# Kernel tuning notes

Measured on AMD Instinct MI355X. Metric: run time of the kernel, lower is better.

Reference implementation:

```python
import jax, jax.numpy as jnp
import numpy as np


def setup_inputs() -> dict:
    key = jax.random.key(0)
    ks = jax.random.split(key, 8)
    B = 32768
    return {
        "x": jax.random.normal(ks[0], (B, 784), dtype=jnp.float32),
        "conv_w": jax.random.normal(ks[1], (3, 3), dtype=jnp.float32),
        "fc1_w": jax.random.normal(ks[2], (512, 676), dtype=jnp.float32) * 0.04,
        "fc1_b": jax.random.normal(ks[3], (512,), dtype=jnp.float32),
        "fc2_w": jax.random.normal(ks[4], (512, 512), dtype=jnp.float32) * 0.04,
        "fc2_b": jax.random.normal(ks[5], (512,), dtype=jnp.float32),
        "out_w": jax.random.normal(ks[6], (10, 512), dtype=jnp.float32) * 0.04,
        "out_b": jax.random.normal(ks[7], (10,), dtype=jnp.float32),
    }


def reference(x, conv_w, fc1_w, fc1_b, fc2_w, fc2_b, out_w, out_b):
    B = x.shape[0]
    img = x.reshape(B, 1, 28, 28)  # NCHW, single channel
    # Valid 3x3 cross-correlation (same math as the nested tensordot loop).
    kern = conv_w.reshape(1, 1, 3, 3)  # OIHW
    conv = jax.lax.conv_general_dilated(
        img, kern, window_strides=(1, 1), padding="VALID",
        dimension_numbers=("NCHW", "OIHW", "NCHW"))  # [B,1,26,26]
    h = conv.reshape(B, 26 * 26)
    h = jax.nn.relu(h @ fc1_w.T + fc1_b)
    h = jax.nn.relu(h @ fc2_w.T + fc2_b)
    return h @ out_w.T + out_b  # [B,10] logits
```

## Files before the change

kernel.cpp:

```cpp
#include <hip/hip_runtime.h>

typedef unsigned short ushort_t;
typedef __attribute__((ext_vector_type(8))) short bf16x8;
typedef __attribute__((ext_vector_type(4))) float f32x4;
typedef __attribute__((ext_vector_type(16))) float f32x16;

__device__ __forceinline__ unsigned short f2bf(float f) {
    union { float f; unsigned u; } v; v.f = f;
    unsigned r = v.u + 0x7FFFu + ((v.u >> 16) & 1u);
    return (unsigned short)(r >> 16);
}

__global__ __launch_bounds__(256) void prep_w(const float* __restrict__ fc1_w,
                                              const float* __restrict__ cw,
                                              const float* __restrict__ fc2_w,
                                              const float* __restrict__ out_w,
                                              ushort_t* __restrict__ W1,
                                              ushort_t* __restrict__ W2,
                                              ushort_t* __restrict__ W3) {
    const int idx = blockIdx.x * 256 + threadIdx.x;
    if (idx < 425984) {
        const int ngrp = idx / 26624;
        const int kfrag = (idx % 26624) >> 9;
        const int li = idx & 511;
        const int lane = li >> 3, e = li & 7;
        const int n = ngrp * 32 + (lane & 31);
        const int p = kfrag * 16 + (lane >> 5) * 8 + e;
        float acc = 0.f;
        if (p < 784) {
            const int pr = p / 28, pc = p % 28;
#pragma unroll
            for (int dr = 0; dr < 3; ++dr) {
                const int r = pr - dr;
                if (r < 0 || r >= 26) continue;
#pragma unroll
                for (int dc = 0; dc < 3; ++dc) {
                    const int col = pc - dc;
                    if (col < 0 || col >= 26) continue;
                    acc += cw[dr * 3 + dc] * fc1_w[n * 676 + r * 26 + col];
                }
            }
        }
        W1[idx] = f2bf(acc);
    }
    if (idx < 262144) {
        const int ngrp = idx / 16384;
        const int kfrag = (idx % 16384) >> 9;
        const int li = idx & 511;
        const int lane = li >> 3, e = li & 7;
        const int n = ngrp * 32 + (lane & 31);
        const int p = kfrag * 16 + (lane >> 5) * 8 + e;
        W2[idx] = f2bf(fc2_w[n * 512 + p]);
    }
    if (idx < 16 * 512)  W3[idx] = (idx < 10 * 512) ? f2bf(out_w[idx]) : (ushort_t)0;
}

__global__ __launch_bounds__(512, 4) void mega5(const float* __restrict__ x,
                                                const ushort_t* __restrict__ W1,
                                                const ushort_t* __restrict__ W2,
                                                const ushort_t* __restrict__ W3,
                                                const float* __restrict__ b1,
                                                const float* __restrict__ b2,
                                                const float* __restrict__ ob,
                                                float* __restrict__ out) {
    extern __shared__ ushort_t smem[];
    ushort_t* xs0 = smem;
    ushort_t* hs  = smem + 4096;

    const int tid = threadIdx.x;
    const int wave = tid >> 6, lane = tid & 63;
    const int r32 = lane & 31, khalf = lane >> 5;
    const int xrow = tid >> 3, xoct = tid & 7;
    const int m0 = blockIdx.x * 64;
    const size_t ng0 = wave * 2, ng1 = wave * 2 + 1;

    f32x16 acc[2][2];
#pragma unroll
    for (int a = 0; a < 2; ++a)
#pragma unroll
        for (int j = 0; j < 2; ++j)
#pragma unroll
            for (int e = 0; e < 16; ++e) acc[a][j][e] = 0.f;

    f32x4 xv0, xv1;
    auto load_x = [&](int ks) {
        const int gc = ks * 64 + xoct * 8;
        if (gc < 784) {
            const f32x4* p = (const f32x4*)&x[(size_t)(m0 + xrow) * 784 + gc];
            xv0 = __builtin_nontemporal_load(p);
            xv1 = __builtin_nontemporal_load(p + 1);
        } else {
            xv0 = (f32x4){0.f, 0.f, 0.f, 0.f};
            xv1 = (f32x4){0.f, 0.f, 0.f, 0.f};
        }
    };
    auto store_x = [&](ushort_t* buf) {
        bf16x8 xv;
        xv[0] = (short)f2bf(xv0.x); xv[1] = (short)f2bf(xv0.y);
        xv[2] = (short)f2bf(xv0.z); xv[3] = (short)f2bf(xv0.w);
        xv[4] = (short)f2bf(xv1.x); xv[5] = (short)f2bf(xv1.y);
        xv[6] = (short)f2bf(xv1.z); xv[7] = (short)f2bf(xv1.w);
        *(bf16x8*)&buf[xrow * 64 + ((xoct ^ (xrow & 7)) * 8)] = xv;
    };

    auto write_h = [&](const float* __restrict__ bias) {
#pragma unroll
        for (int j = 0; j < 2; ++j) {
            const int n = (wave * 2 + j) * 32 + r32;
            const float bb = bias[n];
            const int nseg = n >> 3, nrem = n & 7;
#pragma unroll
            for (int i = 0; i < 2; ++i)
#pragma unroll
                for (int reg = 0; reg < 16; ++reg) {
                    const int m = i * 32 + 4 * khalf + (reg & 3) + 8 * (reg >> 2);
                    hs[m * 512 + ((nseg ^ (m & 7)) * 8) + nrem] = f2bf(fmaxf(acc[i][j][reg] + bb, 0.f));
                }
        }
    };

    load_x(0);
    store_x(xs0);
    __syncthreads();

    for (int ks = 0; ks < 12; ++ks) {
        load_x(ks + 1);
        const ushort_t* bufp = (ks & 1) ? hs : xs0;
#pragma unroll
        for (int ksub = 0; ksub < 4; ++ksub) {
            const int kfrag = ks * 4 + ksub;
            const bf16x8 bw0 = *(const bf16x8*)&W1[(ng0 * 52 + kfrag) * 512 + lane * 8];
            const bf16x8 bw1 = *(const bf16x8*)&W1[(ng1 * 52 + kfrag) * 512 + lane * 8];
            const int q = 2 * ksub + khalf;
            bf16x8 af[2];
#pragma unroll
            for (int i = 0; i < 2; ++i) {
                const int m = i * 32 + r32;
                af[i] = *(const bf16x8*)&bufp[m * 64 + ((q ^ (m & 7)) * 8)];
            }
            __builtin_amdgcn_s_setprio(1);
            acc[0][0] = __builtin_amdgcn_mfma_f32_32x32x16_bf16(af[0], bw0, acc[0][0], 0, 0, 0);
            acc[0][1] = __builtin_amdgcn_mfma_f32_32x32x16_bf16(af[0], bw1, acc[0][1], 0, 0, 0);
            acc[1][0] = __builtin_amdgcn_mfma_f32_32x32x16_bf16(af[1], bw0, acc[1][0], 0, 0, 0);
            acc[1][1] = __builtin_amdgcn_mfma_f32_32x32x16_bf16(af[1], bw1, acc[1][1], 0, 0, 0);
            __builtin_amdgcn_s_setprio(0);
        }
        store_x((ks & 1) ? xs0 : hs);
        __syncthreads();
    }
    {
        const ushort_t* bufp = xs0;
        const int kfrag = 48;
        const bf16x8 bw0 = *(const bf16x8*)&W1[(ng0 * 52 + kfrag) * 512 + lane * 8];
        const bf16x8 bw1 = *(const bf16x8*)&W1[(ng1 * 52 + kfrag) * 512 + lane * 8];
        const int q = khalf;
        bf16x8 af[2];
#pragma unroll
        for (int i = 0; i < 2; ++i) {
            const int m = i * 32 + r32;
            af[i] = *(const bf16x8*)&bufp[m * 64 + ((q ^ (m & 7)) * 8)];
        }
        __builtin_amdgcn_s_setprio(1);
        acc[0][0] = __builtin_amdgcn_mfma_f32_32x32x16_bf16(af[0], bw0, acc[0][0], 0, 0, 0);
        acc[0][1] = __builtin_amdgcn_mfma_f32_32x32x16_bf16(af[0], bw1, acc[0][1], 0, 0, 0);
        acc[1][0] = __builtin_amdgcn_mfma_f32_32x32x16_bf16(af[1], bw0, acc[1][0], 0, 0, 0);
        acc[1][1] = __builtin_amdgcn_mfma_f32_32x32x16_bf16(af[1], bw1, acc[1][1], 0, 0, 0);
        __builtin_amdgcn_s_setprio(0);
    }

    write_h(b1);
#pragma unroll
    for (int a = 0; a < 2; ++a)
#pragma unroll
        for (int j = 0; j < 2; ++j)
#pragma unroll
            for (int e = 0; e < 16; ++e) acc[a][j][e] = 0.f;
    __syncthreads();

    for (int ks = 0; ks < 8; ++ks) {
#pragma unroll
        for (int ksub = 0; ksub < 4; ++ksub) {
            const int kfrag = ks * 4 + ksub;
            const bf16x8 bw0 = *(const bf16x8*)&W2[(ng0 * 32 + kfrag) * 512 + lane * 8];
            const bf16x8 bw1 = *(const bf16x8*)&W2[(ng1 * 32 + kfrag) * 512 + lane * 8];
            const int hq = ks * 8 + 2 * ksub + khalf;
            bf16x8 af[2];
#pragma unroll
            for (int i = 0; i < 2; ++i) {
                const int m = i * 32 + r32;
                af[i] = *(const bf16x8*)&hs[m * 512 + ((hq ^ (m & 7)) * 8)];
            }
            __builtin_amdgcn_s_setprio(1);
            acc[0][0] = __builtin_amdgcn_mfma_f32_32x32x16_bf16(af[0], bw0, acc[0][0], 0, 0, 0);
            acc[0][1] = __builtin_amdgcn_mfma_f32_32x32x16_bf16(af[0], bw1, acc[0][1], 0, 0, 0);
            acc[1][0] = __builtin_amdgcn_mfma_f32_32x32x16_bf16(af[1], bw0, acc[1][0], 0, 0, 0);
            acc[1][1] = __builtin_amdgcn_mfma_f32_32x32x16_bf16(af[1], bw1, acc[1][1], 0, 0, 0);
            __builtin_amdgcn_s_setprio(0);
        }
    }
    __syncthreads();

    write_h(b2);
    __syncthreads();

    if (wave < 4) {
        const int quad = lane >> 4, l16 = lane & 15;
        const int row = wave * 16 + l16;
        f32x4 hacc = {0.f, 0.f, 0.f, 0.f};
#pragma unroll
        for (int ks = 0; ks < 16; ++ks) {
            const int seg = 4 * ks + quad;
            const bf16x8 a = *(const bf16x8*)&hs[row * 512 + ((seg ^ (row & 7)) * 8)];
            const bf16x8 b = *(const bf16x8*)&W3[l16 * 512 + ks * 32 + quad * 8];
            hacc = __builtin_amdgcn_mfma_f32_16x16x32_bf16(a, b, hacc, 0, 0, 0);
        }
        if (l16 < 10) {
            const float bb = ob[l16];
#pragma unroll
            for (int r = 0; r < 4; ++r)
                out[(size_t)(m0 + wave * 16 + quad * 4 + r) * 10 + l16] = hacc[r] + bb;
        }
    }
}

extern "C" void kernel_launch(void* const* d_in, const int* in_sizes, int n_in,
                              void* d_out, int out_size, void* d_ws, size_t ws_size,
                              hipStream_t stream) {
    const float* x      = (const float*)d_in[0];
    const float* conv_w = (const float*)d_in[1];
    const float* fc1_w  = (const float*)d_in[2];
    const float* fc1_b  = (const float*)d_in[3];
    const float* fc2_w  = (const float*)d_in[4];
    const float* fc2_b  = (const float*)d_in[5];
    const float* out_w  = (const float*)d_in[6];
    const float* out_b  = (const float*)d_in[7];
    float* out = (float*)d_out;

    ushort_t* W1 = (ushort_t*)d_ws;
    ushort_t* W2 = W1 + 425984;
    ushort_t* W3 = W2 + 262144;

    prep_w<<<dim3(1664), 256, 0, stream>>>(fc1_w, conv_w, fc2_w, out_w, W1, W2, W3);

    mega5<<<dim3(512), 512, 73728, stream>>>(x, W1, W2, W3, fc1_b, fc2_b, out_b, out);
}
```

Baseline: 216.8 us.

## Double the per-block row tile to 128 and batch weight fragment loads

Each block now processes 128 batch rows instead of 64: 4x2 accumulator tiles per wave, a wider x staging load per thread, double-size LDS buffers, and 256 blocks instead of 512. Every W1/W2 fragment fetched from global memory is reused across twice as many rows, halving total weight traffic. The weight fragments for a k-step are also loaded into registers together before the MFMA loop. The cost is one 144KB-LDS block per CU, meaning fewer resident waves to hide latency, plus much higher register pressure from 128 accumulator floats per lane.

```diff
diff --git a/kernel.cpp b/kernel.cpp
--- a/kernel.cpp
+++ b/kernel.cpp
@@ -55,7 +55,7 @@
     if (idx < 16 * 512)  W3[idx] = (idx < 10 * 512) ? f2bf(out_w[idx]) : (ushort_t)0;
 }
 
-__global__ __launch_bounds__(512, 4) void mega5(const float* __restrict__ x,
+__global__ __launch_bounds__(512, 2) void mega6(const float* __restrict__ x,
                                                 const ushort_t* __restrict__ W1,
                                                 const ushort_t* __restrict__ W2,
                                                 const ushort_t* __restrict__ W3,
@@ -65,42 +65,52 @@
                                                 float* __restrict__ out) {
     extern __shared__ ushort_t smem[];
     ushort_t* xs0 = smem;
-    ushort_t* hs  = smem + 4096;
+    ushort_t* hs  = smem + 8192;
 
     const int tid = threadIdx.x;
     const int wave = tid >> 6, lane = tid & 63;
     const int r32 = lane & 31, khalf = lane >> 5;
-    const int xrow = tid >> 3, xoct = tid & 7;
-    const int m0 = blockIdx.x * 64;
+    const int xrow = tid >> 2, xquad = tid & 3;
+    const int m0 = blockIdx.x * 128;
     const size_t ng0 = wave * 2, ng1 = wave * 2 + 1;
 
-    f32x16 acc[2][2];
-#pragma unroll
-    for (int a = 0; a < 2; ++a)
+    f32x16 acc[4][2];
+#pragma unroll
+    for (int a = 0; a < 4; ++a)
 #pragma unroll
         for (int j = 0; j < 2; ++j)
 #pragma unroll
             for (int e = 0; e < 16; ++e) acc[a][j][e] = 0.f;
 
-    f32x4 xv0, xv1;
+    f32x4 xv0, xv1, xv2, xv3;
     auto load_x = [&](int ks) {
-        const int gc = ks * 64 + xoct * 8;
+        const int gc = ks * 64 + xquad * 16;
         if (gc < 784) {
             const f32x4* p = (const f32x4*)&x[(size_t)(m0 + xrow) * 784 + gc];
             xv0 = __builtin_nontemporal_load(p);
             xv1 = __builtin_nontemporal_load(p + 1);
+            xv2 = __builtin_nontemporal_load(p + 2);
+            xv3 = __builtin_nontemporal_load(p + 3);
         } else {
             xv0 = (f32x4){0.f, 0.f, 0.f, 0.f};
             xv1 = (f32x4){0.f, 0.f, 0.f, 0.f};
+            xv2 = (f32x4){0.f, 0.f, 0.f, 0.f};
+            xv3 = (f32x4){0.f, 0.f, 0.f, 0.f};
         }
     };
     auto store_x = [&](ushort_t* buf) {
-        bf16x8 xv;
-        xv[0] = (short)f2bf(xv0.x); xv[1] = (short)f2bf(xv0.y);
-        xv[2] = (short)f2bf(xv0.z); xv[3] = (short)f2bf(xv0.w);
-        xv[4] = (short)f2bf(xv1.x); xv[5] = (short)f2bf(xv1.y);
-        xv[6] = (short)f2bf(xv1.z); xv[7] = (short)f2bf(xv1.w);
-        *(bf16x8*)&buf[xrow * 64 + ((xoct ^ (xrow & 7)) * 8)] = xv;
+        bf16x8 a, b;
+        a[0] = (short)f2bf(xv0.x); a[1] = (short)f2bf(xv0.y);
+        a[2] = (short)f2bf(xv0.z); a[3] = (short)f2bf(xv0.w);
+        a[4] = (short)f2bf(xv1.x); a[5] = (short)f2bf(xv1.y);
+        a[6] = (short)f2bf(xv1.z); a[7] = (short)f2bf(xv1.w);
+        b[0] = (short)f2bf(xv2.x); b[1] = (short)f2bf(xv2.y);
+        b[2] = (short)f2bf(xv2.z); b[3] = (short)f2bf(xv2.w);
+        b[4] = (short)f2bf(xv3.x); b[5] = (short)f2bf(xv3.y);
+        b[6] = (short)f2bf(xv3.z); b[7] = (short)f2bf(xv3.w);
+        const int o0 = xquad * 2;
+        *(bf16x8*)&buf[xrow * 64 + ((o0 ^ (xrow & 7)) * 8)] = a;
+        *(bf16x8*)&buf[xrow * 64 + (((o0 + 1) ^ (xrow & 7)) * 8)] = b;
     };
 
     auto write_h = [&](const float* __restrict__ bias) {
@@ -110,7 +120,7 @@
             const float bb = bias[n];
             const int nseg = n >> 3, nrem = n & 7;
 #pragma unroll
-            for (int i = 0; i < 2; ++i)
+            for (int i = 0; i < 4; ++i)
 #pragma unroll
                 for (int reg = 0; reg < 16; ++reg) {
                     const int m = i * 32 + 4 * khalf + (reg & 3) + 8 * (reg >> 2);
@@ -124,25 +134,30 @@
     __syncthreads();
 
     for (int ks = 0; ks < 12; ++ks) {
+        bf16x8 bw[4][2];
+#pragma unroll
+        for (int ksub = 0; ksub < 4; ++ksub) {
+            const int kfrag = ks * 4 + ksub;
+            bw[ksub][0] = *(const bf16x8*)&W1[(ng0 * 52 + kfrag) * 512 + lane * 8];
+            bw[ksub][1] = *(const bf16x8*)&W1[(ng1 * 52 + kfrag) * 512 + lane * 8];
+        }
         load_x(ks + 1);
         const ushort_t* bufp = (ks & 1) ? hs : xs0;
 #pragma unroll
         for (int ksub = 0; ksub < 4; ++ksub) {
-            const int kfrag = ks * 4 + ksub;
-            const bf16x8 bw0 = *(const bf16x8*)&W1[(ng0 * 52 + kfrag) * 512 + lane * 8];
-            const bf16x8 bw1 = *(const bf16x8*)&W1[(ng1 * 52 + kfrag) * 512 + lane * 8];
             const int q = 2 * ksub + khalf;
-            bf16x8 af[2];
-#pragma unroll
-            for (int i = 0; i < 2; ++i) {
+            bf16x8 af[4];
+#pragma unroll
+            for (int i = 0; i < 4; ++i) {
                 const int m = i * 32 + r32;
                 af[i] = *(const bf16x8*)&bufp[m * 64 + ((q ^ (m & 7)) * 8)];
             }
             __builtin_amdgcn_s_setprio(1);
-            acc[0][0] = __builtin_amdgcn_mfma_f32_32x32x16_bf16(af[0], bw0, acc[0][0], 0, 0, 0);
-            acc[0][1] = __builtin_amdgcn_mfma_f32_32x32x16_bf16(af[0], bw1, acc[0][1], 0, 0, 0);
-            acc[1][0] = __builtin_amdgcn_mfma_f32_32x32x16_bf16(af[1], bw0, acc[1][0], 0, 0, 0);
-            acc[1][1] = __builtin_amdgcn_mfma_f32_32x32x16_bf16(af[1], bw1, acc[1][1], 0, 0, 0);
+#pragma unroll
+            for (int i = 0; i < 4; ++i) {
+                acc[i][0] = __builtin_amdgcn_mfma_f32_32x32x16_bf16(af[i], bw[ksub][0], acc[i][0], 0, 0, 0);
+                acc[i][1] = __builtin_amdgcn_mfma_f32_32x32x16_bf16(af[i], bw[ksub][1], acc[i][1], 0, 0, 0);
+            }
             __builtin_amdgcn_s_setprio(0);
         }
         store_x((ks & 1) ? xs0 : hs);
@@ -150,27 +165,27 @@
     }
     {
         const ushort_t* bufp = xs0;
-        const int kfrag = 48;
-        const bf16x8 bw0 = *(const bf16x8*)&W1[(ng0 * 52 + kfrag) * 512 + lane * 8];
-        const bf16x8 bw1 = *(const bf16x8*)&W1[(ng1 * 52 + kfrag) * 512 + lane * 8];
+        bf16x8 bw0 = *(const bf16x8*)&W1[(ng0 * 52 + 48) * 512 + lane * 8];
+        bf16x8 bw1 = *(const bf16x8*)&W1[(ng1 * 52 + 48) * 512 + lane * 8];
         const int q = khalf;
-        bf16x8 af[2];
-#pragma unroll
-        for (int i = 0; i < 2; ++i) {
+        bf16x8 af[4];
+#pragma unroll
+        for (int i = 0; i < 4; ++i) {
             const int m = i * 32 + r32;
             af[i] = *(const bf16x8*)&bufp[m * 64 + ((q ^ (m & 7)) * 8)];
         }
         __builtin_amdgcn_s_setprio(1);
-        acc[0][0] = __builtin_amdgcn_mfma_f32_32x32x16_bf16(af[0], bw0, acc[0][0], 0, 0, 0);
-        acc[0][1] = __builtin_amdgcn_mfma_f32_32x32x16_bf16(af[0], bw1, acc[0][1], 0, 0, 0);
-        acc[1][0] = __builtin_amdgcn_mfma_f32_32x32x16_bf16(af[1], bw0, acc[1][0], 0, 0, 0);
-        acc[1][1] = __builtin_amdgcn_mfma_f32_32x32x16_bf16(af[1], bw1, acc[1][1], 0, 0, 0);
+#pragma unroll
+        for (int i = 0; i < 4; ++i) {
+            acc[i][0] = __builtin_amdgcn_mfma_f32_32x32x16_bf16(af[i], bw0, acc[i][0], 0, 0, 0);
+            acc[i][1] = __builtin_amdgcn_mfma_f32_32x32x16_bf16(af[i], bw1, acc[i][1], 0, 0, 0);
+        }
         __builtin_amdgcn_s_setprio(0);
     }
 
     write_h(b1);
 #pragma unroll
-    for (int a = 0; a < 2; ++a)
+    for (int a = 0; a < 4; ++a)
 #pragma unroll
         for (int j = 0; j < 2; ++j)
 #pragma unroll
@@ -178,23 +193,28 @@
     __syncthreads();
 
     for (int ks = 0; ks < 8; ++ks) {
+        bf16x8 bw[4][2];
 #pragma unroll
         for (int ksub = 0; ksub < 4; ++ksub) {
             const int kfrag = ks * 4 + ksub;
-            const bf16x8 bw0 = *(const bf16x8*)&W2[(ng0 * 32 + kfrag) * 512 + lane * 8];
-            const bf16x8 bw1 = *(const bf16x8*)&W2[(ng1 * 32 + kfrag) * 512 + lane * 8];
+            bw[ksub][0] = *(const bf16x8*)&W2[(ng0 * 32 + kfrag) * 512 + lane * 8];
+            bw[ksub][1] = *(const bf16x8*)&W2[(ng1 * 32 + kfrag) * 512 + lane * 8];
+        }
+#pragma unroll
+        for (int ksub = 0; ksub < 4; ++ksub) {
             const int hq = ks * 8 + 2 * ksub + khalf;
-            bf16x8 af[2];
-#pragma unroll
-            for (int i = 0; i < 2; ++i) {
+            bf16x8 af[4];
+#pragma unroll
+            for (int i = 0; i < 4; ++i) {
                 const int m = i * 32 + r32;
                 af[i] = *(const bf16x8*)&hs[m * 512 + ((hq ^ (m & 7)) * 8)];
             }
             __builtin_amdgcn_s_setprio(1);
-            acc[0][0] = __builtin_amdgcn_mfma_f32_32x32x16_bf16(af[0], bw0, acc[0][0], 0, 0, 0);
-            acc[0][1] = __builtin_amdgcn_mfma_f32_32x32x16_bf16(af[0], bw1, acc[0][1], 0, 0, 0);
-            acc[1][0] = __builtin_amdgcn_mfma_f32_32x32x16_bf16(af[1], bw0, acc[1][0], 0, 0, 0);
-            acc[1][1] = __builtin_amdgcn_mfma_f32_32x32x16_bf16(af[1], bw1, acc[1][1], 0, 0, 0);
+#pragma unroll
+            for (int i = 0; i < 4; ++i) {
+                acc[i][0] = __builtin_amdgcn_mfma_f32_32x32x16_bf16(af[i], bw[ksub][0], acc[i][0], 0, 0, 0);
+                acc[i][1] = __builtin_amdgcn_mfma_f32_32x32x16_bf16(af[i], bw[ksub][1], acc[i][1], 0, 0, 0);
+            }
             __builtin_amdgcn_s_setprio(0);
         }
     }
@@ -203,7 +223,7 @@
     write_h(b2);
     __syncthreads();
 
-    if (wave < 4) {
+    {
         const int quad = lane >> 4, l16 = lane & 15;
         const int row = wave * 16 + l16;
         f32x4 hacc = {0.f, 0.f, 0.f, 0.f};
@@ -242,5 +262,5 @@
 
     prep_w<<<dim3(1664), 256, 0, stream>>>(fc1_w, conv_w, fc2_w, out_w, W1, W2, W3);
 
-    mega5<<<dim3(512), 512, 73728, stream>>>(x, W1, W2, W3, fc1_b, fc2_b, out_b, out);
-}
+    mega6<<<dim3(256), 512, 147456, stream>>>(x, W1, W2, W3, fc1_b, fc2_b, out_b, out);
+}
```

New measurement: 228.9 us. +5.6%, slower.

## Double block to 128 rows with 1024 threads, load x directly into MFMA fragments

Applied to the files above, without the earlier changes.

The fused MLP kernel now handles 128 rows per block using 16 waves, two groups of 8 along M sharing each weight tile. The x staging through LDS and its per-step barriers are removed: each lane loads its fp32 A-fragment straight from global memory and converts it with the packed bf16 convert instruction. This cuts LDS traffic and synchronisation and halves the number of blocks. In exchange the x loads become strided per-lane fp32 reads with no prefetch, the block needs 128KB of LDS, and only 256 blocks are launched.

```diff
diff --git a/kernel.cpp b/kernel.cpp
--- a/kernel.cpp
+++ b/kernel.cpp
@@ -9,6 +9,12 @@
     union { float f; unsigned u; } v; v.f = f;
     unsigned r = v.u + 0x7FFFu + ((v.u >> 16) & 1u);
     return (unsigned short)(r >> 16);
+}
+
+__device__ __forceinline__ unsigned cvt_pk_bf16(float a, float b) {
+    unsigned r;
+    asm("v_cvt_pk_bf16_f32 %0, %1, %2" : "=v"(r) : "v"(a), "v"(b));
+    return r;
 }
 
 __global__ __launch_bounds__(256) void prep_w(const float* __restrict__ fc1_w,
@@ -55,24 +61,27 @@
     if (idx < 16 * 512)  W3[idx] = (idx < 10 * 512) ? f2bf(out_w[idx]) : (ushort_t)0;
 }
 
-__global__ __launch_bounds__(512, 4) void mega5(const float* __restrict__ x,
-                                                const ushort_t* __restrict__ W1,
-                                                const ushort_t* __restrict__ W2,
-                                                const ushort_t* __restrict__ W3,
-                                                const float* __restrict__ b1,
-                                                const float* __restrict__ b2,
-                                                const float* __restrict__ ob,
-                                                float* __restrict__ out) {
+__global__ __launch_bounds__(1024, 4) void mega7(const float* __restrict__ x,
+                                                 const ushort_t* __restrict__ W1,
+                                                 const ushort_t* __restrict__ W2,
+                                                 const ushort_t* __restrict__ W3,
+                                                 const float* __restrict__ b1,
+                                                 const float* __restrict__ b2,
+                                                 const float* __restrict__ ob,
+                                                 float* __restrict__ out) {
     extern __shared__ ushort_t smem[];
-    ushort_t* xs0 = smem;
-    ushort_t* hs  = smem + 4096;
+    ushort_t* hs = smem;
 
     const int tid = threadIdx.x;
     const int wave = tid >> 6, lane = tid & 63;
     const int r32 = lane & 31, khalf = lane >> 5;
-    const int xrow = tid >> 3, xoct = tid & 7;
-    const int m0 = blockIdx.x * 64;
-    const size_t ng0 = wave * 2, ng1 = wave * 2 + 1;
+    const int wm = wave >> 3;
+    const int wn = wave & 7;
+    const size_t ng0 = wn * 2, ng1 = wn * 2 + 1;
+    const int m0 = blockIdx.x * 128;
+
+    const float* xr0 = x + (size_t)(m0 + wm * 64 + r32) * 784 + khalf * 8;
+    const float* xr1 = xr0 + (size_t)32 * 784;
 
     f32x16 acc[2][2];
 #pragma unroll
@@ -82,89 +91,60 @@
 #pragma unroll
             for (int e = 0; e < 16; ++e) acc[a][j][e] = 0.f;
 
-    f32x4 xv0, xv1;
-    auto load_x = [&](int ks) {
-        const int gc = ks * 64 + xoct * 8;
-        if (gc < 784) {
-            const f32x4* p = (const f32x4*)&x[(size_t)(m0 + xrow) * 784 + gc];
-            xv0 = __builtin_nontemporal_load(p);
-            xv1 = __builtin_nontemporal_load(p + 1);
-        } else {
-            xv0 = (f32x4){0.f, 0.f, 0.f, 0.f};
-            xv1 = (f32x4){0.f, 0.f, 0.f, 0.f};
-        }
+    auto mk_af = [&](const float* xr, int kf) -> bf16x8 {
+        const f32x4 a = *(const f32x4*)(xr + kf * 16);
+        const f32x4 b = *(const f32x4*)(xr + kf * 16 + 4);
+        union { bf16x8 h; unsigned u[4]; } r;
+        r.u[0] = cvt_pk_bf16(a.x, a.y);
+        r.u[1] = cvt_pk_bf16(a.z, a.w);
+        r.u[2] = cvt_pk_bf16(b.x, b.y);
+        r.u[3] = cvt_pk_bf16(b.z, b.w);
+        return r.h;
     };
-    auto store_x = [&](ushort_t* buf) {
-        bf16x8 xv;
-        xv[0] = (short)f2bf(xv0.x); xv[1] = (short)f2bf(xv0.y);
-        xv[2] = (short)f2bf(xv0.z); xv[3] = (short)f2bf(xv0.w);
-        xv[4] = (short)f2bf(xv1.x); xv[5] = (short)f2bf(xv1.y);
-        xv[6] = (short)f2bf(xv1.z); xv[7] = (short)f2bf(xv1.w);
-        *(bf16x8*)&buf[xrow * 64 + ((xoct ^ (xrow & 7)) * 8)] = xv;
-    };
 
     auto write_h = [&](const float* __restrict__ bias) {
 #pragma unroll
         for (int j = 0; j < 2; ++j) {
-            const int n = (wave * 2 + j) * 32 + r32;
+            const int n = (wn * 2 + j) * 32 + r32;
             const float bb = bias[n];
             const int nseg = n >> 3, nrem = n & 7;
 #pragma unroll
             for (int i = 0; i < 2; ++i)
 #pragma unroll
                 for (int reg = 0; reg < 16; ++reg) {
-                    const int m = i * 32 + 4 * khalf + (reg & 3) + 8 * (reg >> 2);
+                    const int m = wm * 64 + i * 32 + 4 * khalf + (reg & 3) + 8 * (reg >> 2);
                     hs[m * 512 + ((nseg ^ (m & 7)) * 8) + nrem] = f2bf(fmaxf(acc[i][j][reg] + bb, 0.f));
                 }
         }
     };
 
-    load_x(0);
-    store_x(xs0);
-    __syncthreads();
-
     for (int ks = 0; ks < 12; ++ks) {
-        load_x(ks + 1);
-        const ushort_t* bufp = (ks & 1) ? hs : xs0;
 #pragma unroll
         for (int ksub = 0; ksub < 4; ++ksub) {
-            const int kfrag = ks * 4 + ksub;
-            const bf16x8 bw0 = *(const bf16x8*)&W1[(ng0 * 52 + kfrag) * 512 + lane * 8];
-            const bf16x8 bw1 = *(const bf16x8*)&W1[(ng1 * 52 + kfrag) * 512 + lane * 8];
-            const int q = 2 * ksub + khalf;
-            bf16x8 af[2];
-#pragma unroll
-            for (int i = 0; i < 2; ++i) {
-                const int m = i * 32 + r32;
-                af[i] = *(const bf16x8*)&bufp[m * 64 + ((q ^ (m & 7)) * 8)];
-            }
+            const int kf = ks * 4 + ksub;
+            const bf16x8 bw0 = *(const bf16x8*)&W1[(ng0 * 52 + kf) * 512 + lane * 8];
+            const bf16x8 bw1 = *(const bf16x8*)&W1[(ng1 * 52 + kf) * 512 + lane * 8];
+            const bf16x8 af0 = mk_af(xr0, kf);
+            const bf16x8 af1 = mk_af(xr1, kf);
             __builtin_amdgcn_s_setprio(1);
-            acc[0][0] = __builtin_amdgcn_mfma_f32_32x32x16_bf16(af[0], bw0, acc[0][0], 0, 0, 0);
-            acc[0][1] = __builtin_amdgcn_mfma_f32_32x32x16_bf16(af[0], bw1, acc[0][1], 0, 0, 0);
-            acc[1][0] = __builtin_amdgcn_mfma_f32_32x32x16_bf16(af[1], bw0, acc[1][0], 0, 0, 0);
-            acc[1][1] = __builtin_amdgcn_mfma_f32_32x32x16_bf16(af[1], bw1, acc[1][1], 0, 0, 0);
+            acc[0][0] = __builtin_amdgcn_mfma_f32_32x32x16_bf16(af0, bw0, acc[0][0], 0, 0, 0);
+            acc[0][1] = __builtin_amdgcn_mfma_f32_32x32x16_bf16(af0, bw1, acc[0][1], 0, 0, 0);
+            acc[1][0] = __builtin_amdgcn_mfma_f32_32x32x16_bf16(af1, bw0, acc[1][0], 0, 0, 0);
+            acc[1][1] = __builtin_amdgcn_mfma_f32_32x32x16_bf16(af1, bw1, acc[1][1], 0, 0, 0);
             __builtin_amdgcn_s_setprio(0);
         }
-        store_x((ks & 1) ? xs0 : hs);
-        __syncthreads();
     }
     {
-        const ushort_t* bufp = xs0;
-        const int kfrag = 48;
-        const bf16x8 bw0 = *(const bf16x8*)&W1[(ng0 * 52 + kfrag) * 512 + lane * 8];
-        const bf16x8 bw1 = *(const bf16x8*)&W1[(ng1 * 52 + kfrag) * 512 + lane * 8];
-        const int q = khalf;
-        bf16x8 af[2];
-#pragma unroll
-        for (int i = 0; i < 2; ++i) {
-            const int m = i * 32 + r32;
-            af[i] = *(const bf16x8*)&bufp[m * 64 + ((q ^ (m & 7)) * 8)];
-        }
+        const int kf = 48;
+        const bf16x8 bw0 = *(const bf16x8*)&W1[(ng0 * 52 + kf) * 512 + lane * 8];
+        const bf16x8 bw1 = *(const bf16x8*)&W1[(ng1 * 52 + kf) * 512 + lane * 8];
+        const bf16x8 af0 = mk_af(xr0, kf);
+        const bf16x8 af1 = mk_af(xr1, kf);
         __builtin_amdgcn_s_setprio(1);
-        acc[0][0] = __builtin_amdgcn_mfma_f32_32x32x16_bf16(af[0], bw0, acc[0][0], 0, 0, 0);
-        acc[0][1] = __builtin_amdgcn_mfma_f32_32x32x16_bf16(af[0], bw1, acc[0][1], 0, 0, 0);
-        acc[1][0] = __builtin_amdgcn_mfma_f32_32x32x16_bf16(af[1], bw0, acc[1][0], 0, 0, 0);
-        acc[1][1] = __builtin_amdgcn_mfma_f32_32x32x16_bf16(af[1], bw1, acc[1][1], 0, 0, 0);
+        acc[0][0] = __builtin_amdgcn_mfma_f32_32x32x16_bf16(af0, bw0, acc[0][0], 0, 0, 0);
+        acc[0][1] = __builtin_amdgcn_mfma_f32_32x32x16_bf16(af0, bw1, acc[0][1], 0, 0, 0);
+        acc[1][0] = __builtin_amdgcn_mfma_f32_32x32x16_bf16(af1, bw0, acc[1][0], 0, 0, 0);
+        acc[1][1] = __builtin_amdgcn_mfma_f32_32x32x16_bf16(af1, bw1, acc[1][1], 0, 0, 0);
         __builtin_amdgcn_s_setprio(0);
     }
 
@@ -180,14 +160,14 @@
     for (int ks = 0; ks < 8; ++ks) {
 #pragma unroll
         for (int ksub = 0; ksub < 4; ++ksub) {
-            const int kfrag = ks * 4 + ksub;
-            const bf16x8 bw0 = *(const bf16x8*)&W2[(ng0 * 32 + kfrag) * 512 + lane * 8];
-            const bf16x8 bw1 = *(const bf16x8*)&W2[(ng1 * 32 + kfrag) * 512 + lane * 8];
-            const int hq = ks * 8 + 2 * ksub + khalf;
+            const int kf = ks * 4 + ksub;
+            const bf16x8 bw0 = *(const bf16x8*)&W2[(ng0 * 32 + kf) * 512 + lane * 8];
+            const bf16x8 bw1 = *(const bf16x8*)&W2[(ng1 * 32 + kf) * 512 + lane * 8];
+            const int hq = kf * 2 + khalf;
             bf16x8 af[2];
 #pragma unroll
             for (int i = 0; i < 2; ++i) {
-                const int m = i * 32 + r32;
+                const int m = wm * 64 + i * 32 + r32;
                 af[i] = *(const bf16x8*)&hs[m * 512 + ((hq ^ (m & 7)) * 8)];
             }
             __builtin_amdgcn_s_setprio(1);
@@ -203,7 +183,7 @@
     write_h(b2);
     __syncthreads();
 
-    if (wave < 4) {
+    if (wave < 8) {
         const int quad = lane >> 4, l16 = lane & 15;
         const int row = wave * 16 + l16;
         f32x4 hacc = {0.f, 0.f, 0.f, 0.f};
@@ -242,5 +222,5 @@
 
     prep_w<<<dim3(1664), 256, 0, stream>>>(fc1_w, conv_w, fc2_w, out_w, W1, W2, W3);
 
-    mega5<<<dim3(512), 512, 73728, stream>>>(x, W1, W2, W3, fc1_b, fc2_b, out_b, out);
-}
+    mega7<<<dim3(256), 1024, 131072, stream>>>(x, W1, W2, W3, fc1_b, fc2_b, out_b, out);
+}
```

Result: slower. 257.0 us (+18.5%).

## Split N-groups across 16 waves per block instead of 8

Applied to the files above, without the earlier changes.

Doubles the block to 1024 threads so each wave computes one 32-column N-group instead of two, halving accumulator registers per wave. Only the first 512 threads stage the x tile. This aims to raise wave-level parallelism and latency hiding on the MFMA pipelines, at the cost of re-reading A fragments from LDS twice as often and heavier barriers.

```diff
diff --git a/kernel.cpp b/kernel.cpp
--- a/kernel.cpp
+++ b/kernel.cpp
@@ -55,14 +55,14 @@
     if (idx < 16 * 512)  W3[idx] = (idx < 10 * 512) ? f2bf(out_w[idx]) : (ushort_t)0;
 }
 
-__global__ __launch_bounds__(512, 4) void mega5(const float* __restrict__ x,
-                                                const ushort_t* __restrict__ W1,
-                                                const ushort_t* __restrict__ W2,
-                                                const ushort_t* __restrict__ W3,
-                                                const float* __restrict__ b1,
-                                                const float* __restrict__ b2,
-                                                const float* __restrict__ ob,
-                                                float* __restrict__ out) {
+__global__ __launch_bounds__(1024, 4) void mega8(const float* __restrict__ x,
+                                                 const ushort_t* __restrict__ W1,
+                                                 const ushort_t* __restrict__ W2,
+                                                 const ushort_t* __restrict__ W3,
+                                                 const float* __restrict__ b1,
+                                                 const float* __restrict__ b2,
+                                                 const float* __restrict__ ob,
+                                                 float* __restrict__ out) {
     extern __shared__ ushort_t smem[];
     ushort_t* xs0 = smem;
     ushort_t* hs  = smem + 4096;
@@ -70,17 +70,16 @@
     const int tid = threadIdx.x;
     const int wave = tid >> 6, lane = tid & 63;
     const int r32 = lane & 31, khalf = lane >> 5;
+    const bool stager = tid < 512;
     const int xrow = tid >> 3, xoct = tid & 7;
     const int m0 = blockIdx.x * 64;
-    const size_t ng0 = wave * 2, ng1 = wave * 2 + 1;
-
-    f32x16 acc[2][2];
+    const size_t ng = wave;
+
+    f32x16 acc[2];
 #pragma unroll
     for (int a = 0; a < 2; ++a)
 #pragma unroll
-        for (int j = 0; j < 2; ++j)
-#pragma unroll
-            for (int e = 0; e < 16; ++e) acc[a][j][e] = 0.f;
+        for (int e = 0; e < 16; ++e) acc[a][e] = 0.f;
 
     f32x4 xv0, xv1;
     auto load_x = [&](int ks) {
@@ -104,33 +103,28 @@
     };
 
     auto write_h = [&](const float* __restrict__ bias) {
-#pragma unroll
-        for (int j = 0; j < 2; ++j) {
-            const int n = (wave * 2 + j) * 32 + r32;
-            const float bb = bias[n];
-            const int nseg = n >> 3, nrem = n & 7;
-#pragma unroll
-            for (int i = 0; i < 2; ++i)
-#pragma unroll
-                for (int reg = 0; reg < 16; ++reg) {
-                    const int m = i * 32 + 4 * khalf + (reg & 3) + 8 * (reg >> 2);
-                    hs[m * 512 + ((nseg ^ (m & 7)) * 8) + nrem] = f2bf(fmaxf(acc[i][j][reg] + bb, 0.f));
-                }
-        }
+        const int n = wave * 32 + r32;
+        const float bb = bias[n];
+        const int nseg = n >> 3, nrem = n & 7;
+#pragma unroll
+        for (int i = 0; i < 2; ++i)
+#pragma unroll
+            for (int reg = 0; reg < 16; ++reg) {
+                const int m = i * 32 + 4 * khalf + (reg & 3) + 8 * (reg >> 2);
+                hs[m * 512 + ((nseg ^ (m & 7)) * 8) + nrem] = f2bf(fmaxf(acc[i][reg] + bb, 0.f));
+            }
     };
 
-    load_x(0);
-    store_x(xs0);
+    if (stager) { load_x(0); store_x(xs0); }
     __syncthreads();
 
     for (int ks = 0; ks < 12; ++ks) {
-        load_x(ks + 1);
+        if (stager) load_x(ks + 1);
         const ushort_t* bufp = (ks & 1) ? hs : xs0;
 #pragma unroll
         for (int ksub = 0; ksub < 4; ++ksub) {
-            const int kfrag = ks * 4 + ksub;
-            const bf16x8 bw0 = *(const bf16x8*)&W1[(ng0 * 52 + kfrag) * 512 + lane * 8];
-            const bf16x8 bw1 = *(const bf16x8*)&W1[(ng1 * 52 + kfrag) * 512 + lane * 8];
+            const int kf = ks * 4 + ksub;
+            const bf16x8 bw = *(const bf16x8*)&W1[(ng * 52 + kf) * 512 + lane * 8];
             const int q = 2 * ksub + khalf;
             bf16x8 af[2];
 #pragma unroll
@@ -139,20 +133,16 @@
                 af[i] = *(const bf16x8*)&bufp[m * 64 + ((q ^ (m & 7)) * 8)];
             }
             __builtin_amdgcn_s_setprio(1);
-            acc[0][0] = __builtin_amdgcn_mfma_f32_32x32x16_bf16(af[0], bw0, acc[0][0], 0, 0, 0);
-            acc[0][1] = __builtin_amdgcn_mfma_f32_32x32x16_bf16(af[0], bw1, acc[0][1], 0, 0, 0);
-            acc[1][0] = __builtin_amdgcn_mfma_f32_32x32x16_bf16(af[1], bw0, acc[1][0], 0, 0, 0);
-            acc[1][1] = __builtin_amdgcn_mfma_f32_32x32x16_bf16(af[1], bw1, acc[1][1], 0, 0, 0);
+            acc[0] = __builtin_amdgcn_mfma_f32_32x32x16_bf16(af[0], bw, acc[0], 0, 0, 0);
+            acc[1] = __builtin_amdgcn_mfma_f32_32x32x16_bf16(af[1], bw, acc[1], 0, 0, 0);
             __builtin_amdgcn_s_setprio(0);
         }
-        store_x((ks & 1) ? xs0 : hs);
+        if (stager) store_x((ks & 1) ? xs0 : hs);
         __syncthreads();
     }
     {
         const ushort_t* bufp = xs0;
-        const int kfrag = 48;
-        const bf16x8 bw0 = *(const bf16x8*)&W1[(ng0 * 52 + kfrag) * 512 + lane * 8];
-        const bf16x8 bw1 = *(const bf16x8*)&W1[(ng1 * 52 + kfrag) * 512 + lane * 8];
+        const bf16x8 bw = *(const bf16x8*)&W1[(ng * 52 + 48) * 512 + lane * 8];
         const int q = khalf;
         bf16x8 af[2];
 #pragma unroll
@@ -161,10 +151,8 @@
             af[i] = *(const bf16x8*)&bufp[m * 64 + ((q ^ (m & 7)) * 8)];
         }
         __builtin_amdgcn_s_setprio(1);
-        acc[0][0] = __builtin_amdgcn_mfma_f32_32x32x16_bf16(af[0], bw0, acc[0][0], 0, 0, 0);
-        acc[0][1] = __builtin_amdgcn_mfma_f32_32x32x16_bf16(af[0], bw1, acc[0][1], 0, 0, 0);
-        acc[1][0] = __builtin_amdgcn_mfma_f32_32x32x16_bf16(af[1], bw0, acc[1][0], 0, 0, 0);
-        acc[1][1] = __builtin_amdgcn_mfma_f32_32x32x16_bf16(af[1], bw1, acc[1][1], 0, 0, 0);
+        acc[0] = __builtin_amdgcn_mfma_f32_32x32x16_bf16(af[0], bw, acc[0], 0, 0, 0);
+        acc[1] = __builtin_amdgcn_mfma_f32_32x32x16_bf16(af[1], bw, acc[1], 0, 0, 0);
         __builtin_amdgcn_s_setprio(0);
     }
 
@@ -172,18 +160,15 @@
 #pragma unroll
     for (int a = 0; a < 2; ++a)
 #pragma unroll
-        for (int j = 0; j < 2; ++j)
-#pragma unroll
-            for (int e = 0; e < 16; ++e) acc[a][j][e] = 0.f;
+        for (int e = 0; e < 16; ++e) acc[a][e] = 0.f;
     __syncthreads();
 
     for (int ks = 0; ks < 8; ++ks) {
 #pragma unroll
         for (int ksub = 0; ksub < 4; ++ksub) {
-            const int kfrag = ks * 4 + ksub;
-            const bf16x8 bw0 = *(const bf16x8*)&W2[(ng0 * 32 + kfrag) * 512 + lane * 8];
-            const bf16x8 bw1 = *(const bf16x8*)&W2[(ng1 * 32 + kfrag) * 512 + lane * 8];
-            const int hq = ks * 8 + 2 * ksub + khalf;
+            const int kf = ks * 4 + ksub;
+            const bf16x8 bw = *(const bf16x8*)&W2[(ng * 32 + kf) * 512 + lane * 8];
+            const int hq = kf * 2 + khalf;
             bf16x8 af[2];
 #pragma unroll
             for (int i = 0; i < 2; ++i) {
@@ -191,10 +176,8 @@
                 af[i] = *(const bf16x8*)&hs[m * 512 + ((hq ^ (m & 7)) * 8)];
             }
             __builtin_amdgcn_s_setprio(1);
-            acc[0][0] = __builtin_amdgcn_mfma_f32_32x32x16_bf16(af[0], bw0, acc[0][0], 0, 0, 0);
-            acc[0][1] = __builtin_amdgcn_mfma_f32_32x32x16_bf16(af[0], bw1, acc[0][1], 0, 0, 0);
-            acc[1][0] = __builtin_amdgcn_mfma_f32_32x32x16_bf16(af[1], bw0, acc[1][0], 0, 0, 0);
-            acc[1][1] = __builtin_amdgcn_mfma_f32_32x32x16_bf16(af[1], bw1, acc[1][1], 0, 0, 0);
+            acc[0] = __builtin_amdgcn_mfma_f32_32x32x16_bf16(af[0], bw, acc[0], 0, 0, 0);
+            acc[1] = __builtin_amdgcn_mfma_f32_32x32x16_bf16(af[1], bw, acc[1], 0, 0, 0);
             __builtin_amdgcn_s_setprio(0);
         }
     }
@@ -242,5 +225,5 @@
 
     prep_w<<<dim3(1664), 256, 0, stream>>>(fc1_w, conv_w, fc2_w, out_w, W1, W2, W3);
 
-    mega5<<<dim3(512), 512, 73728, stream>>>(x, W1, W2, W3, fc1_b, fc2_b, out_b, out);
-}
+    mega8<<<dim3(512), 1024, 73728, stream>>>(x, W1, W2, W3, fc1_b, fc2_b, out_b, out);
+}
```

Result: no change. 218.7 us (+0.9%).
